# Performance work log

Hardware: AMD Instinct MI355X
Metric: run time of the kernel (lower is better)

Reference implementation:

```python
import jax, jax.numpy as jnp
import numpy as np

G, N, E = 64, 2048, 32768      # graphs, nodes/graph, edges/graph
D, H, O, L = 128, 128, 2, 3    # node_dim, hid_dim, out_dim, max_layer
ALL = 500_000                  # global feature table rows


def setup_inputs() -> dict:
    key = jax.random.key(0)
    ks = jax.random.split(key, 12)
    s = 1.0 / np.sqrt(D)  # D == H so one scale suffices
    return {
        "all_features": jax.random.normal(ks[0], (ALL, D), jnp.float32),
        "feature_index": jax.random.randint(ks[1], (G, N), 0, ALL),
        "edge_index": jax.random.randint(ks[2], (G, 2, E), 0, N),
        "action": 2,  # uses action+1 = 3 GCN layers
        "lin_res_w": jax.random.normal(ks[3], (D, H), jnp.float32) * s,
        "lin_res_b": jnp.zeros((H,), jnp.float32),
        "gcn_w": jax.random.normal(ks[4], (L, H, H), jnp.float32) * s,
        "gcn_b": jnp.zeros((L, H), jnp.float32),
        "fc1_w": jax.random.normal(ks[5], (H, H), jnp.float32) * s,
        "fc1_b": jnp.zeros((H,), jnp.float32),
        "lin_w": jax.random.normal(ks[6], (H, O), jnp.float32) * s,
        "lin_b": jnp.zeros((O,), jnp.float32),
    }


def _gcn_conv(x, src, dst, W, b):
    """PyG GCNConv: add self-loops, symmetric deg^-1/2 norm, scatter-add."""
    n = x.shape[0]
    h = x @ W                                             # [N,H]
    loop = jnp.arange(n)
    src2 = jnp.concatenate([src, loop])
    dst2 = jnp.concatenate([dst, loop])
    deg = jax.ops.segment_sum(jnp.ones_like(dst2, dtype=h.dtype), dst2,
                              num_segments=n)             # >=1 via self-loops
    dinv = jax.lax.rsqrt(deg)
    coef = dinv[src2] * dinv[dst2]                        # [E+N]
    out = jax.ops.segment_sum(h[src2] * coef[:, None], dst2, num_segments=n)
    return out + b


def reference(all_features, feature_index, edge_index, action,
              lin_res_w, lin_res_b, gcn_w, gcn_b,
              fc1_w, fc1_b, lin_w, lin_b):
    n_layers = int(action) + 1

    def per_graph(feats, src, dst):
        # residual branch (dropout is identity in eval mode)
        x1 = jax.nn.relu(feats @ lin_res_w + lin_res_b)   # [N,H]
        x = feats
        for k in range(n_layers):
            x = jax.nn.relu(_gcn_conv(x, src, dst, gcn_w[k], gcn_b[k]))
        x = jax.nn.relu((x + x1) @ fc1_w + fc1_b)
        return jnp.mean(x, axis=0)                        # [H]

    feats = all_features[feature_index]                   # [G,N,D] gather
    target_feats = jax.vmap(per_graph)(feats, edge_index[:, 0], edge_index[:, 1])
    logits = target_feats @ lin_w + lin_b                 # [G,O]
    return jax.nn.log_softmax(logits, axis=1), logits
```

## Files before the change

kernel.cpp:

```cpp
#include <hip/hip_runtime.h>

#define G 64
#define N 2048
#define E 32768
#define GN (G*N)
#define PADR 36

typedef __attribute__((ext_vector_type(8))) short bf16x8;
typedef __attribute__((ext_vector_type(4))) float f32x4;

__device__ __forceinline__ float4 ld4(const float* p) { return *reinterpret_cast<const float4*>(p); }
__device__ __forceinline__ unsigned short f2bf(float x) {
    unsigned u = __float_as_uint(x);
    u += 0x7FFF + ((u >> 16) & 1);
    return (unsigned short)(u >> 16);
}
__device__ __forceinline__ unsigned pack2(float a, float b) {
    return (unsigned)f2bf(a) | ((unsigned)f2bf(b) << 16);
}
__device__ __forceinline__ float bflo(unsigned u) { return __uint_as_float(u << 16); }
__device__ __forceinline__ float bfhi(unsigned u) { return __uint_as_float(u & 0xFFFF0000u); }
__device__ __forceinline__ float bfs(short s) { return __uint_as_float(((unsigned)(unsigned short)s) << 16); }

__device__ __forceinline__ int swz(int bid, int chunk) { return (bid & 7) * chunk + (bid >> 3); }

__global__ __launch_bounds__(1024) void k_init(const int* __restrict__ ei,
        float* __restrict__ dinv, int* __restrict__ perm, int* __restrict__ rankg,
        int* __restrict__ sdeg, float* __restrict__ sdinv, int* __restrict__ lvlG,
        const float* __restrict__ wres, const float* __restrict__ gw,
        const float* __restrict__ wfc, unsigned short* __restrict__ Wt,
        float* __restrict__ tgt) {
    int t = threadIdx.x;
    if (blockIdx.x == G + 40) {
        #pragma unroll
        for (int j = 0; j < 8; ++j) tgt[j*1024 + t] = 0.f;
        return;
    }
    if (blockIdx.x >= G) {
        if (t >= 256) return;
        int pb = blockIdx.x - G;
        int m = pb >> 3;
        int tid = (pb & 7) * 256 + t;
        const float* src = (m == 0) ? wres : (m < 4 ? gw + (size_t)(m-1)*16384 : wfc);
        int c = tid >> 4, q = tid & 15;
        float v[8];
        #pragma unroll
        for (int j = 0; j < 8; ++j) v[j] = src[(q*8 + j)*128 + c];
        uint4 p;
        p.x = pack2(v[0], v[1]); p.y = pack2(v[2], v[3]);
        p.z = pack2(v[4], v[5]); p.w = pack2(v[6], v[7]);
        *reinterpret_cast<uint4*>(Wt + (size_t)m*16384 + c*128 + ((q ^ (c & 7)) << 3)) = p;
        return;
    }
    int g = blockIdx.x;
    __shared__ int scnt[2048];
    __shared__ int hist[128];
    __shared__ int basev[129];
    __shared__ int lvl[128];
    __shared__ int ctr[128];
    scnt[t] = 0; scnt[t + 1024] = 0;
    if (t < 128) { hist[t] = 0; ctr[t] = 0; }
    __syncthreads();
    const int* dstp = ei + (size_t)g*2*E + E;
    for (int e = t; e < E; e += 1024) atomicAdd(&scnt[dstp[e]], 1);
    __syncthreads();
    int a = scnt[2*t], b = scnt[2*t + 1];
    dinv[(g<<11) + 2*t]     = rsqrtf((float)(a + 1));
    dinv[(g<<11) + 2*t + 1] = rsqrtf((float)(b + 1));
    int ba = min(a, 127), bb = min(b, 127);
    atomicAdd(&hist[ba], 1);
    atomicAdd(&hist[bb], 1);
    __syncthreads();
    if (t == 0) {
        int suf = 0;
        basev[128] = 0;
        for (int d = 127; d >= 0; --d) { suf += hist[d]; basev[d] = suf; }
        int run = 0;
        for (int i = 0; i < 128; ++i) { lvl[i] = run; run += basev[i + 1]; }
    }
    __syncthreads();
    {
        int sa = basev[ba + 1] + atomicAdd(&ctr[ba], 1);
        perm[(g<<11) + sa] = 2*t;
        sdeg[(g<<11) + sa] = a;
        sdinv[(g<<11) + sa] = rsqrtf((float)(a + 1));
        rankg[(g<<11) + 2*t] = sa;
        int sb = basev[bb + 1] + atomicAdd(&ctr[bb], 1);
        perm[(g<<11) + sb] = 2*t + 1;
        sdeg[(g<<11) + sb] = b;
        sdinv[(g<<11) + sb] = rsqrtf((float)(b + 1));
        rankg[(g<<11) + 2*t + 1] = sb;
    }
    if (t < 128) lvlG[g*128 + t] = lvl[t];
}

__global__ __launch_bounds__(512) void k_gemm_g2(const int* __restrict__ fidx,
        const float* __restrict__ tab, const unsigned short* __restrict__ Wt,
        const float* __restrict__ bres, const float* __restrict__ dinv,
        unsigned short* __restrict__ X1, unsigned short* __restrict__ Hb,
        const int* __restrict__ ei, const int* __restrict__ rankg,
        const int* __restrict__ lvlG, int* __restrict__ padj) {
    __shared__ unsigned short sW[2*16384];
    const int t = threadIdx.x;

    if (blockIdx.x < G) {
        int* cur   = reinterpret_cast<int*>(sW);
        int* rankL = cur + 2048;
        int* lvlL  = rankL + 2048;
        int g = blockIdx.x;
        #pragma unroll
        for (int i = 0; i < 4; ++i) {
            cur[i*512 + t] = 0;
            rankL[i*512 + t] = rankg[(g<<11) + i*512 + t];
        }
        if (t < 128) lvlL[t] = lvlG[g*128 + t];
        __syncthreads();
        const int* srcp = ei + (size_t)g*2*E;
        const int* dstp = srcp + E;
        for (int e = t; e < E; e += 512) {
            int dst = dstp[e];
            int i = atomicAdd(&cur[dst], 1);
            padj[(size_t)g*E + lvlL[i] + rankL[dst]] = srcp[e];
        }
        return;
    }

    {
        const float4* s = reinterpret_cast<const float4*>(Wt);
        float4* d = reinterpret_cast<float4*>(sW);
        #pragma unroll
        for (int i = 0; i < 8; ++i) d[i*512 + t] = s[i*512 + t];
    }
    __syncthreads();

    const int lane = t & 63, w = t >> 6;
    const int wrow = (w & 3) << 6;
    const int wcol = (w >> 2) << 6;
    const size_t row0 = (size_t)swz(blockIdx.x - G, GN/256/8) * 256;
    const int l15 = lane & 15, l4 = lane >> 4;

    size_t rbase[4];
    const float* rowp[4];
    #pragma unroll
    for (int f2 = 0; f2 < 4; ++f2) {
        rbase[f2] = row0 + wrow + f2*16 + l15;
        rowp[f2] = tab + (size_t)fidx[rbase[f2]] * 128;
    }

    f32x4 acc0[4][4], acc1[4][4];
    #pragma unroll
    for (int i = 0; i < 4; ++i)
        #pragma unroll
        for (int j = 0; j < 4; ++j) {
            acc0[i][j] = (f32x4){0.f, 0.f, 0.f, 0.f};
            acc1[i][j] = (f32x4){0.f, 0.f, 0.f, 0.f};
        }

    #pragma unroll
    for (int kk = 0; kk < 4; ++kk) {
        bf16x8 xf[4];
        #pragma unroll
        for (int f2 = 0; f2 < 4; ++f2) {
            int col = (kk << 5) + (l4 << 3);
            float4 u = ld4(rowp[f2] + col);
            float4 v = ld4(rowp[f2] + col + 4);
            bf16x8 r;
            r[0] = (short)f2bf(u.x); r[1] = (short)f2bf(u.y);
            r[2] = (short)f2bf(u.z); r[3] = (short)f2bf(u.w);
            r[4] = (short)f2bf(v.x); r[5] = (short)f2bf(v.y);
            r[6] = (short)f2bf(v.z); r[7] = (short)f2bf(v.w);
            xf[f2] = r;
        }
        #pragma unroll
        for (int f = 0; f < 4; ++f) {
            int c = wcol + f*16 + l15;
            int off = c*128 + (((kk*4 + l4) ^ (c & 7)) << 3);
            bf16x8 wf0 = *reinterpret_cast<const bf16x8*>(&sW[off]);
            bf16x8 wf1 = *reinterpret_cast<const bf16x8*>(&sW[16384 + off]);
            #pragma unroll
            for (int f2 = 0; f2 < 4; ++f2) {
                acc0[f2][f] = __builtin_amdgcn_mfma_f32_16x16x32_bf16(wf0, xf[f2], acc0[f2][f], 0, 0, 0);
                acc1[f2][f] = __builtin_amdgcn_mfma_f32_16x16x32_bf16(wf1, xf[f2], acc1[f2][f], 0, 0, 0);
            }
        }
    }

    float dv[4];
    #pragma unroll
    for (int f2 = 0; f2 < 4; ++f2) dv[f2] = dinv[rbase[f2]];

    #pragma unroll
    for (int f = 0; f < 4; ++f) {
        int colb = wcol + f*16 + (l4 << 2);
        float4 bs = ld4(bres + colb);
        #pragma unroll
        for (int f2 = 0; f2 < 4; ++f2) {
            f32x4 v0 = acc0[f2][f];
            uint2 p0;
            p0.x = pack2(fmaxf(v0[0] + bs.x, 0.f), fmaxf(v0[1] + bs.y, 0.f));
            p0.y = pack2(fmaxf(v0[2] + bs.z, 0.f), fmaxf(v0[3] + bs.w, 0.f));
            *reinterpret_cast<uint2*>(X1 + (rbase[f2] << 7) + colb) = p0;
            f32x4 v1 = acc1[f2][f];
            float d = dv[f2];
            uint2 p1;
            p1.x = pack2(v1[0]*d, v1[1]*d);
            p1.y = pack2(v1[2]*d, v1[3]*d);
            *reinterpret_cast<uint2*>(Hb + (rbase[f2] << 7) + colb) = p1;
        }
    }
}

template<int MODE>
__global__ __launch_bounds__(512) void k_gemm(const unsigned short* __restrict__ A,
        const unsigned short* __restrict__ A2, const unsigned short* __restrict__ Wt,
        const float* __restrict__ bias, const float* __restrict__ dinv,
        unsigned short* __restrict__ C, float* __restrict__ tgt) {
    __shared__ unsigned short sW[16384];
    const int t = threadIdx.x;
    {
        const float4* s = reinterpret_cast<const float4*>(Wt);
        float4* d = reinterpret_cast<float4*>(sW);
        #pragma unroll
        for (int i = 0; i < 4; ++i) d[i*512 + t] = s[i*512 + t];
    }
    __syncthreads();

    const int lane = t & 63, w = t >> 6;
    const int wrow = (w & 3) << 6;
    const int wcol = (w >> 2) << 6;
    const size_t row0 = (size_t)swz(blockIdx.x, GN/256/8) * 256;
    const int l15 = lane & 15, l4 = lane >> 4;

    size_t rbase[4];
    #pragma unroll
    for (int f2 = 0; f2 < 4; ++f2) rbase[f2] = row0 + wrow + f2*16 + l15;

    f32x4 acc[4][4];
    #pragma unroll
    for (int i = 0; i < 4; ++i)
        #pragma unroll
        for (int j = 0; j < 4; ++j) acc[i][j] = (f32x4){0.f, 0.f, 0.f, 0.f};

    #pragma unroll
    for (int kk = 0; kk < 4; ++kk) {
        bf16x8 xf[4];
        #pragma unroll
        for (int f2 = 0; f2 < 4; ++f2) {
            const unsigned short* ap = A + (rbase[f2] << 7) + (kk << 5) + (l4 << 3);
            if (MODE == 2) {
                bf16x8 x = *reinterpret_cast<const bf16x8*>(ap);
                bf16x8 y = *reinterpret_cast<const bf16x8*>(A2 + (rbase[f2] << 7) + (kk << 5) + (l4 << 3));
                bf16x8 r;
                #pragma unroll
                for (int j = 0; j < 8; ++j) r[j] = (short)f2bf(bfs(x[j]) + bfs(y[j]));
                xf[f2] = r;
            } else {
                xf[f2] = *reinterpret_cast<const bf16x8*>(ap);
            }
        }
        #pragma unroll
        for (int f = 0; f < 4; ++f) {
            int c = wcol + f*16 + l15;
            int off = c*128 + (((kk*4 + l4) ^ (c & 7)) << 3);
            bf16x8 wf = *reinterpret_cast<const bf16x8*>(&sW[off]);
            #pragma unroll
            for (int f2 = 0; f2 < 4; ++f2)
                acc[f2][f] = __builtin_amdgcn_mfma_f32_16x16x32_bf16(wf, xf[f2], acc[f2][f], 0, 0, 0);
        }
    }

    if (MODE == 2) {
        float cs[4][4];
        #pragma unroll
        for (int f = 0; f < 4; ++f) {
            int colb = wcol + f*16 + (l4 << 2);
            float4 bs = ld4(bias + colb);
            #pragma unroll
            for (int j = 0; j < 4; ++j) cs[f][j] = 0.f;
            #pragma unroll
            for (int f2 = 0; f2 < 4; ++f2) {
                cs[f][0] += fmaxf(acc[f2][f][0] + bs.x, 0.f);
                cs[f][1] += fmaxf(acc[f2][f][1] + bs.y, 0.f);
                cs[f][2] += fmaxf(acc[f2][f][2] + bs.z, 0.f);
                cs[f][3] += fmaxf(acc[f2][f][3] + bs.w, 0.f);
            }
        }
        #pragma unroll
        for (int d = 1; d < 16; d <<= 1)
            #pragma unroll
            for (int f = 0; f < 4; ++f)
                #pragma unroll
                for (int j = 0; j < 4; ++j)
                    cs[f][j] += __shfl_xor(cs[f][j], d);
        if (l15 == 0) {
            int g = (int)(row0 >> 11);
            #pragma unroll
            for (int f = 0; f < 4; ++f)
                #pragma unroll
                for (int j = 0; j < 4; ++j)
                    atomicAdd(&tgt[g*128 + wcol + f*16 + (l4 << 2) + j], cs[f][j]);
        }
        return;
    }

    float dv[4];
    #pragma unroll
    for (int f2 = 0; f2 < 4; ++f2) dv[f2] = dinv[rbase[f2]];
    #pragma unroll
    for (int f = 0; f < 4; ++f) {
        int colb = wcol + f*16 + (l4 << 2);
        #pragma unroll
        for (int f2 = 0; f2 < 4; ++f2) {
            f32x4 v = acc[f2][f];
            float d = dv[f2];
            uint2 p; p.x = pack2(v[0]*d, v[1]*d); p.y = pack2(v[2]*d, v[3]*d);
            *reinterpret_cast<uint2*>(C + (rbase[f2] << 7) + colb) = p;
        }
    }
}

__global__ __launch_bounds__(1024) void k_agg(const unsigned short* __restrict__ h,
        const int* __restrict__ padj, const int* __restrict__ lvlG,
        const int* __restrict__ perm, const int* __restrict__ sdeg,
        const float* __restrict__ sdinv, const float* __restrict__ bias,
        unsigned short* __restrict__ out) {
    __shared__ unsigned short sIN[2048 * PADR];
    __shared__ int lvlL[128];
    const int t = threadIdx.x;
    const int g  = blockIdx.x >> 2;
    const int c0 = (blockIdx.x & 3) << 5;
    const unsigned short* hg = h + (((size_t)g << 11) << 7) + c0;

    if (t < 128) lvlL[t] = lvlG[g*128 + t];
    {
        int r0 = t >> 3;
        int j  = t & 7;
        for (int i = 0; i < 16; ++i) {
            int r = r0 + (i << 7);
            uint2 v = *reinterpret_cast<const uint2*>(hg + ((size_t)r << 7) + j*4);
            *reinterpret_cast<uint2*>(&sIN[r*PADR + j*4]) = v;
        }
    }
    __syncthreads();

    const int* pa = padj + (size_t)g*E;
    float bs[32];
    #pragma unroll
    for (int q = 0; q < 8; ++q) {
        float4 b4 = ld4(bias + c0 + q*4);
        bs[q*4] = b4.x; bs[q*4+1] = b4.y; bs[q*4+2] = b4.z; bs[q*4+3] = b4.w;
    }

    #pragma unroll
    for (int half = 0; half < 2; ++half) {
        const int r = t + (half << 10);
        const int n  = perm[(g << 11) + r];
        const int dg = sdeg[(g << 11) + r];
        const float dv = sdinv[(g << 11) + r];
        float acc[32];
        {
            const unsigned short* rp = &sIN[n*PADR];
            #pragma unroll
            for (int q = 0; q < 8; ++q) {
                uint2 u = *reinterpret_cast<const uint2*>(rp + q*4);
                acc[q*4]   = bflo(u.x); acc[q*4+1] = bfhi(u.x);
                acc[q*4+2] = bflo(u.y); acc[q*4+3] = bfhi(u.y);
            }
        }
        int i = 0;
        for (; i + 2 <= dg; i += 2) {
            int s0 = pa[lvlL[i] + r];
            int s1 = pa[lvlL[i+1] + r];
            const unsigned short* rp0 = &sIN[s0*PADR];
            const unsigned short* rp1 = &sIN[s1*PADR];
            uint2 u0[8], u1[8];
            #pragma unroll
            for (int q = 0; q < 8; ++q) u0[q] = *reinterpret_cast<const uint2*>(rp0 + q*4);
            #pragma unroll
            for (int q = 0; q < 8; ++q) u1[q] = *reinterpret_cast<const uint2*>(rp1 + q*4);
            #pragma unroll
            for (int q = 0; q < 8; ++q) {
                acc[q*4]   += bflo(u0[q].x) + bflo(u1[q].x);
                acc[q*4+1] += bfhi(u0[q].x) + bfhi(u1[q].x);
                acc[q*4+2] += bflo(u0[q].y) + bflo(u1[q].y);
                acc[q*4+3] += bfhi(u0[q].y) + bfhi(u1[q].y);
            }
        }
        if (i < dg) {
            int s = pa[lvlL[i] + r];
            const unsigned short* rp = &sIN[s*PADR];
            #pragma unroll
            for (int q = 0; q < 8; ++q) {
                uint2 u = *reinterpret_cast<const uint2*>(rp + q*4);
                acc[q*4]   += bflo(u.x); acc[q*4+1] += bfhi(u.x);
                acc[q*4+2] += bflo(u.y); acc[q*4+3] += bfhi(u.y);
            }
        }
        unsigned short* op = out + (((size_t)(g << 11) + n) << 7) + c0;
        uint4 o0, o1;
        o0.x = pack2(fmaxf(acc[0]*dv+bs[0],0.f),  fmaxf(acc[1]*dv+bs[1],0.f));
        o0.y = pack2(fmaxf(acc[2]*dv+bs[2],0.f),  fmaxf(acc[3]*dv+bs[3],0.f));
        o0.z = pack2(fmaxf(acc[4]*dv+bs[4],0.f),  fmaxf(acc[5]*dv+bs[5],0.f));
        o0.w = pack2(fmaxf(acc[6]*dv+bs[6],0.f),  fmaxf(acc[7]*dv+bs[7],0.f));
        o1.x = pack2(fmaxf(acc[8]*dv+bs[8],0.f),  fmaxf(acc[9]*dv+bs[9],0.f));
        o1.y = pack2(fmaxf(acc[10]*dv+bs[10],0.f),fmaxf(acc[11]*dv+bs[11],0.f));
        o1.z = pack2(fmaxf(acc[12]*dv+bs[12],0.f),fmaxf(acc[13]*dv+bs[13],0.f));
        o1.w = pack2(fmaxf(acc[14]*dv+bs[14],0.f),fmaxf(acc[15]*dv+bs[15],0.f));
        *reinterpret_cast<uint4*>(op) = o0;
        *reinterpret_cast<uint4*>(op + 8) = o1;
        uint4 o2, o3;
        o2.x = pack2(fmaxf(acc[16]*dv+bs[16],0.f),fmaxf(acc[17]*dv+bs[17],0.f));
        o2.y = pack2(fmaxf(acc[18]*dv+bs[18],0.f),fmaxf(acc[19]*dv+bs[19],0.f));
        o2.z = pack2(fmaxf(acc[20]*dv+bs[20],0.f),fmaxf(acc[21]*dv+bs[21],0.f));
        o2.w = pack2(fmaxf(acc[22]*dv+bs[22],0.f),fmaxf(acc[23]*dv+bs[23],0.f));
        o3.x = pack2(fmaxf(acc[24]*dv+bs[24],0.f),fmaxf(acc[25]*dv+bs[25],0.f));
        o3.y = pack2(fmaxf(acc[26]*dv+bs[26],0.f),fmaxf(acc[27]*dv+bs[27],0.f));
        o3.z = pack2(fmaxf(acc[28]*dv+bs[28],0.f),fmaxf(acc[29]*dv+bs[29],0.f));
        o3.w = pack2(fmaxf(acc[30]*dv+bs[30],0.f),fmaxf(acc[31]*dv+bs[31],0.f));
        *reinterpret_cast<uint4*>(op + 16) = o2;
        *reinterpret_cast<uint4*>(op + 24) = o3;
    }
}

__global__ __launch_bounds__(64) void k_final(const float* __restrict__ tgt,
        const float* __restrict__ lw, const float* __restrict__ lb, float* __restrict__ outp) {
    int g = blockIdx.x, lane = threadIdx.x;
    float l0 = 0.f, l1 = 0.f;
    #pragma unroll
    for (int c = lane; c < 128; c += 64) {
        float v = tgt[g*128 + c] * (1.0f/2048.0f);
        l0 += v * lw[c*2];
        l1 += v * lw[c*2 + 1];
    }
    #pragma unroll
    for (int d = 32; d; d >>= 1) { l0 += __shfl_xor(l0, d); l1 += __shfl_xor(l1, d); }
    if (lane == 0) {
        l0 += lb[0]; l1 += lb[1];
        float m = fmaxf(l0, l1);
        float lse = m + logf(expf(l0 - m) + expf(l1 - m));
        outp[g*2]         = l0 - lse;
        outp[g*2 + 1]     = l1 - lse;
        outp[G*2 + g*2]     = l0;
        outp[G*2 + g*2 + 1] = l1;
    }
}

extern "C" void kernel_launch(void* const* d_in, const int* in_sizes, int n_in,
                              void* d_out, int out_size, void* d_ws, size_t ws_size,
                              hipStream_t stream) {
    const float* all_features = (const float*)d_in[0];
    const int*   fidx = (const int*)d_in[1];
    const int*   ei   = (const int*)d_in[2];
    const float* wres = (const float*)d_in[4];
    const float* bres = (const float*)d_in[5];
    const float* gw   = (const float*)d_in[6];
    const float* gb   = (const float*)d_in[7];
    const float* wfc  = (const float*)d_in[8];
    const float* bfc  = (const float*)d_in[9];
    const float* lw   = (const float*)d_in[10];
    const float* lb   = (const float*)d_in[11];
    float* out = (float*)d_out;

    char* ws = (char*)d_ws;
    size_t o = 0;
    auto alloc = [&](size_t bytes) { char* p = ws + o; o += (bytes + 255) & ~(size_t)255; return p; };
    unsigned short* X  = (unsigned short*)alloc((size_t)GN*128*2);
    unsigned short* Hb = (unsigned short*)alloc((size_t)GN*128*2);
    unsigned short* X1 = (unsigned short*)alloc((size_t)GN*128*2);
    unsigned short* Wt = (unsigned short*)alloc((size_t)5*16384*2);
    int*   padj  = (int*)alloc((size_t)G*E*4);
    int*   lvlG  = (int*)alloc((size_t)G*128*4);
    int*   perm  = (int*)alloc((size_t)GN*4);
    int*   rankg = (int*)alloc((size_t)GN*4);
    int*   sdeg  = (int*)alloc((size_t)GN*4);
    float* sdinv = (float*)alloc((size_t)GN*4);
    float* dinv  = (float*)alloc((size_t)GN*4);
    float* tgt   = (float*)alloc((size_t)G*128*4);

    k_init<<<G + 41, 1024, 0, stream>>>(ei, dinv, perm, rankg, sdeg, sdinv, lvlG,
                                        wres, gw, wfc, Wt, tgt);

    k_gemm_g2<<<G + GN/256, 512, 0, stream>>>(fidx, all_features, Wt, bres, dinv, X1, Hb,
                                              ei, rankg, lvlG, padj);

    k_agg<<<G*4, 1024, 0, stream>>>(Hb, padj, lvlG, perm, sdeg, sdinv, gb, X);
    for (int l = 1; l < 3; ++l) {
        k_gemm<1><<<GN/256, 512, 0, stream>>>(X, nullptr, Wt + (size_t)(1+l)*16384, nullptr, dinv, Hb, nullptr);
        k_agg<<<G*4, 1024, 0, stream>>>(Hb, padj, lvlG, perm, sdeg, sdinv, gb + (size_t)l*128, X);
    }

    k_gemm<2><<<GN/256, 512, 0, stream>>>(X, X1, Wt + (size_t)4*16384, bfc, nullptr, nullptr, tgt);

    k_final<<<G, 64, 0, stream>>>(tgt, lw, lb, out);
}
```

Baseline: 268.8 us.

## Fuse per-layer GEMM into GCN aggregation kernel for layers two and three

Each block now multiplies its graph's full node tile by a 32-column slice of the layer weight using MFMA, scales by dinv and writes the result straight into the shared-memory staging buffer. It then runs the neighbour aggregation from LDS, so the separate GEMM kernel and its global write and read of the hidden tensor disappear for layers 2 and 3. The trade-off is that each of the four column blocks per graph reads the whole input row set (4x redundant X reads) and holds fewer rows per MFMA wave. Launch count drops by two.

```diff
diff --git a/kernel.cpp b/kernel.cpp
--- a/kernel.cpp
+++ b/kernel.cpp
@@ -210,11 +210,9 @@
     }
 }
 
-template<int MODE>
-__global__ __launch_bounds__(512) void k_gemm(const unsigned short* __restrict__ A,
+__global__ __launch_bounds__(512) void k_gemm2(const unsigned short* __restrict__ A,
         const unsigned short* __restrict__ A2, const unsigned short* __restrict__ Wt,
-        const float* __restrict__ bias, const float* __restrict__ dinv,
-        unsigned short* __restrict__ C, float* __restrict__ tgt) {
+        const float* __restrict__ bias, float* __restrict__ tgt) {
     __shared__ unsigned short sW[16384];
     const int t = threadIdx.x;
     {
@@ -247,16 +245,12 @@
         #pragma unroll
         for (int f2 = 0; f2 < 4; ++f2) {
             const unsigned short* ap = A + (rbase[f2] << 7) + (kk << 5) + (l4 << 3);
-            if (MODE == 2) {
-                bf16x8 x = *reinterpret_cast<const bf16x8*>(ap);
-                bf16x8 y = *reinterpret_cast<const bf16x8*>(A2 + (rbase[f2] << 7) + (kk << 5) + (l4 << 3));
-                bf16x8 r;
-                #pragma unroll
-                for (int j = 0; j < 8; ++j) r[j] = (short)f2bf(bfs(x[j]) + bfs(y[j]));
-                xf[f2] = r;
-            } else {
-                xf[f2] = *reinterpret_cast<const bf16x8*>(ap);
-            }
+            bf16x8 x = *reinterpret_cast<const bf16x8*>(ap);
+            bf16x8 y = *reinterpret_cast<const bf16x8*>(A2 + (rbase[f2] << 7) + (kk << 5) + (l4 << 3));
+            bf16x8 r;
+            #pragma unroll
+            for (int j = 0; j < 8; ++j) r[j] = (short)f2bf(bfs(x[j]) + bfs(y[j]));
+            xf[f2] = r;
         }
         #pragma unroll
         for (int f = 0; f < 4; ++f) {
@@ -269,53 +263,35 @@
         }
     }
 
-    if (MODE == 2) {
-        float cs[4][4];
-        #pragma unroll
-        for (int f = 0; f < 4; ++f) {
-            int colb = wcol + f*16 + (l4 << 2);
-            float4 bs = ld4(bias + colb);
-            #pragma unroll
-            for (int j = 0; j < 4; ++j) cs[f][j] = 0.f;
-            #pragma unroll
-            for (int f2 = 0; f2 < 4; ++f2) {
-                cs[f][0] += fmaxf(acc[f2][f][0] + bs.x, 0.f);
-                cs[f][1] += fmaxf(acc[f2][f][1] + bs.y, 0.f);
-                cs[f][2] += fmaxf(acc[f2][f][2] + bs.z, 0.f);
-                cs[f][3] += fmaxf(acc[f2][f][3] + bs.w, 0.f);
-            }
-        }
-        #pragma unroll
-        for (int d = 1; d < 16; d <<= 1)
-            #pragma unroll
-            for (int f = 0; f < 4; ++f)
-                #pragma unroll
-                for (int j = 0; j < 4; ++j)
-                    cs[f][j] += __shfl_xor(cs[f][j], d);
-        if (l15 == 0) {
-            int g = (int)(row0 >> 11);
-            #pragma unroll
-            for (int f = 0; f < 4; ++f)
-                #pragma unroll
-                for (int j = 0; j < 4; ++j)
-                    atomicAdd(&tgt[g*128 + wcol + f*16 + (l4 << 2) + j], cs[f][j]);
-        }
-        return;
-    }
-
-    float dv[4];
-    #pragma unroll
-    for (int f2 = 0; f2 < 4; ++f2) dv[f2] = dinv[rbase[f2]];
+    float cs[4][4];
     #pragma unroll
     for (int f = 0; f < 4; ++f) {
         int colb = wcol + f*16 + (l4 << 2);
+        float4 bs = ld4(bias + colb);
+        #pragma unroll
+        for (int j = 0; j < 4; ++j) cs[f][j] = 0.f;
         #pragma unroll
         for (int f2 = 0; f2 < 4; ++f2) {
-            f32x4 v = acc[f2][f];
-            float d = dv[f2];
-            uint2 p; p.x = pack2(v[0]*d, v[1]*d); p.y = pack2(v[2]*d, v[3]*d);
-            *reinterpret_cast<uint2*>(C + (rbase[f2] << 7) + colb) = p;
-        }
+            cs[f][0] += fmaxf(acc[f2][f][0] + bs.x, 0.f);
+            cs[f][1] += fmaxf(acc[f2][f][1] + bs.y, 0.f);
+            cs[f][2] += fmaxf(acc[f2][f][2] + bs.z, 0.f);
+            cs[f][3] += fmaxf(acc[f2][f][3] + bs.w, 0.f);
+        }
+    }
+    #pragma unroll
+    for (int d = 1; d < 16; d <<= 1)
+        #pragma unroll
+        for (int f = 0; f < 4; ++f)
+            #pragma unroll
+            for (int j = 0; j < 4; ++j)
+                cs[f][j] += __shfl_xor(cs[f][j], d);
+    if (l15 == 0) {
+        int g = (int)(row0 >> 11);
+        #pragma unroll
+        for (int f = 0; f < 4; ++f)
+            #pragma unroll
+            for (int j = 0; j < 4; ++j)
+                atomicAdd(&tgt[g*128 + wcol + f*16 + (l4 << 2) + j], cs[f][j]);
     }
 }
 
@@ -422,6 +398,135 @@
     }
 }
 
+__global__ __launch_bounds__(1024) void k_fused(const unsigned short* __restrict__ Xin,
+        const unsigned short* __restrict__ WtL,
+        const int* __restrict__ padj, const int* __restrict__ lvlG,
+        const int* __restrict__ perm, const int* __restrict__ sdeg,
+        const float* __restrict__ sdinv, const float* __restrict__ dinv,
+        const float* __restrict__ bias,
+        unsigned short* __restrict__ Xout) {
+    __shared__ unsigned short sIN[2048 * PADR];
+    __shared__ int lvlL[128];
+    const int t = threadIdx.x;
+    const int wg = swz(blockIdx.x, 32);
+    const int g  = wg >> 2;
+    const int c0 = (wg & 3) << 5;
+
+    if (t < 128) lvlL[t] = lvlG[g*128 + t];
+
+    const int lane = t & 63, wv = t >> 6;
+    const int l15 = lane & 15, l4 = lane >> 4;
+
+    bf16x8 wf[2][4];
+    #pragma unroll
+    for (int f = 0; f < 2; ++f) {
+        int c = c0 + f*16 + l15;
+        #pragma unroll
+        for (int kk = 0; kk < 4; ++kk)
+            wf[f][kk] = *reinterpret_cast<const bf16x8*>(&WtL[c*128 + (((kk*4 + l4) ^ (c & 7)) << 3)]);
+    }
+
+    const unsigned short* xg = Xin + (((size_t)g << 11) << 7);
+    #pragma unroll
+    for (int rt = 0; rt < 8; ++rt) {
+        int rowb = ((wv << 3) + rt) << 4;
+        int row = rowb + l15;
+        f32x4 acc0 = (f32x4){0.f,0.f,0.f,0.f};
+        f32x4 acc1 = (f32x4){0.f,0.f,0.f,0.f};
+        #pragma unroll
+        for (int kk = 0; kk < 4; ++kk) {
+            bf16x8 xf = *reinterpret_cast<const bf16x8*>(xg + ((size_t)row << 7) + (kk << 5) + (l4 << 3));
+            acc0 = __builtin_amdgcn_mfma_f32_16x16x32_bf16(wf[0][kk], xf, acc0, 0, 0, 0);
+            acc1 = __builtin_amdgcn_mfma_f32_16x16x32_bf16(wf[1][kk], xf, acc1, 0, 0, 0);
+        }
+        float d = dinv[(g << 11) + row];
+        uint2 p0, p1;
+        p0.x = pack2(acc0[0]*d, acc0[1]*d); p0.y = pack2(acc0[2]*d, acc0[3]*d);
+        p1.x = pack2(acc1[0]*d, acc1[1]*d); p1.y = pack2(acc1[2]*d, acc1[3]*d);
+        *reinterpret_cast<uint2*>(&sIN[row*PADR + (l4 << 2)])      = p0;
+        *reinterpret_cast<uint2*>(&sIN[row*PADR + 16 + (l4 << 2)]) = p1;
+    }
+    __syncthreads();
+
+    const int* pa = padj + (size_t)g*E;
+    float bs[32];
+    #pragma unroll
+    for (int q = 0; q < 8; ++q) {
+        float4 b4 = ld4(bias + c0 + q*4);
+        bs[q*4] = b4.x; bs[q*4+1] = b4.y; bs[q*4+2] = b4.z; bs[q*4+3] = b4.w;
+    }
+
+    #pragma unroll
+    for (int half = 0; half < 2; ++half) {
+        const int r = t + (half << 10);
+        const int n  = perm[(g << 11) + r];
+        const int dg = sdeg[(g << 11) + r];
+        const float dv = sdinv[(g << 11) + r];
+        float acc[32];
+        {
+            const unsigned short* rp = &sIN[n*PADR];
+            #pragma unroll
+            for (int q = 0; q < 8; ++q) {
+                uint2 u = *reinterpret_cast<const uint2*>(rp + q*4);
+                acc[q*4]   = bflo(u.x); acc[q*4+1] = bfhi(u.x);
+                acc[q*4+2] = bflo(u.y); acc[q*4+3] = bfhi(u.y);
+            }
+        }
+        int i = 0;
+        for (; i + 2 <= dg; i += 2) {
+            int s0 = pa[lvlL[i] + r];
+            int s1 = pa[lvlL[i+1] + r];
+            const unsigned short* rp0 = &sIN[s0*PADR];
+            const unsigned short* rp1 = &sIN[s1*PADR];
+            uint2 u0[8], u1[8];
+            #pragma unroll
+            for (int q = 0; q < 8; ++q) u0[q] = *reinterpret_cast<const uint2*>(rp0 + q*4);
+            #pragma unroll
+            for (int q = 0; q < 8; ++q) u1[q] = *reinterpret_cast<const uint2*>(rp1 + q*4);
+            #pragma unroll
+            for (int q = 0; q < 8; ++q) {
+                acc[q*4]   += bflo(u0[q].x) + bflo(u1[q].x);
+                acc[q*4+1] += bfhi(u0[q].x) + bfhi(u1[q].x);
+                acc[q*4+2] += bflo(u0[q].y) + bflo(u1[q].y);
+                acc[q*4+3] += bfhi(u0[q].y) + bfhi(u1[q].y);
+            }
+        }
+        if (i < dg) {
+            int s = pa[lvlL[i] + r];
+            const unsigned short* rp = &sIN[s*PADR];
+            #pragma unroll
+            for (int q = 0; q < 8; ++q) {
+                uint2 u = *reinterpret_cast<const uint2*>(rp + q*4);
+                acc[q*4]   += bflo(u.x); acc[q*4+1] += bfhi(u.x);
+                acc[q*4+2] += bflo(u.y); acc[q*4+3] += bfhi(u.y);
+            }
+        }
+        unsigned short* op = Xout + (((size_t)(g << 11) + n) << 7) + c0;
+        uint4 o0, o1;
+        o0.x = pack2(fmaxf(acc[0]*dv+bs[0],0.f),  fmaxf(acc[1]*dv+bs[1],0.f));
+        o0.y = pack2(fmaxf(acc[2]*dv+bs[2],0.f),  fmaxf(acc[3]*dv+bs[3],0.f));
+        o0.z = pack2(fmaxf(acc[4]*dv+bs[4],0.f),  fmaxf(acc[5]*dv+bs[5],0.f));
+        o0.w = pack2(fmaxf(acc[6]*dv+bs[6],0.f),  fmaxf(acc[7]*dv+bs[7],0.f));
+        o1.x = pack2(fmaxf(acc[8]*dv+bs[8],0.f),  fmaxf(acc[9]*dv+bs[9],0.f));
+        o1.y = pack2(fmaxf(acc[10]*dv+bs[10],0.f),fmaxf(acc[11]*dv+bs[11],0.f));
+        o1.z = pack2(fmaxf(acc[12]*dv+bs[12],0.f),fmaxf(acc[13]*dv+bs[13],0.f));
+        o1.w = pack2(fmaxf(acc[14]*dv+bs[14],0.f),fmaxf(acc[15]*dv+bs[15],0.f));
+        *reinterpret_cast<uint4*>(op) = o0;
+        *reinterpret_cast<uint4*>(op + 8) = o1;
+        uint4 o2, o3;
+        o2.x = pack2(fmaxf(acc[16]*dv+bs[16],0.f),fmaxf(acc[17]*dv+bs[17],0.f));
+        o2.y = pack2(fmaxf(acc[18]*dv+bs[18],0.f),fmaxf(acc[19]*dv+bs[19],0.f));
+        o2.z = pack2(fmaxf(acc[20]*dv+bs[20],0.f),fmaxf(acc[21]*dv+bs[21],0.f));
+        o2.w = pack2(fmaxf(acc[22]*dv+bs[22],0.f),fmaxf(acc[23]*dv+bs[23],0.f));
+        o3.x = pack2(fmaxf(acc[24]*dv+bs[24],0.f),fmaxf(acc[25]*dv+bs[25],0.f));
+        o3.y = pack2(fmaxf(acc[26]*dv+bs[26],0.f),fmaxf(acc[27]*dv+bs[27],0.f));
+        o3.z = pack2(fmaxf(acc[28]*dv+bs[28],0.f),fmaxf(acc[29]*dv+bs[29],0.f));
+        o3.w = pack2(fmaxf(acc[30]*dv+bs[30],0.f),fmaxf(acc[31]*dv+bs[31],0.f));
+        *reinterpret_cast<uint4*>(op + 16) = o2;
+        *reinterpret_cast<uint4*>(op + 24) = o3;
+    }
+}
+
 __global__ __launch_bounds__(64) void k_final(const float* __restrict__ tgt,
         const float* __restrict__ lw, const float* __restrict__ lb, float* __restrict__ outp) {
     int g = blockIdx.x, lane = threadIdx.x;
@@ -465,7 +570,7 @@
     size_t o = 0;
     auto alloc = [&](size_t bytes) { char* p = ws + o; o += (bytes + 255) & ~(size_t)255; return p; };
     unsigned short* X  = (unsigned short*)alloc((size_t)GN*128*2);
-    unsigned short* Hb = (unsigned short*)alloc((size_t)GN*128*2);
+    unsigned short* Xb = (unsigned short*)alloc((size_t)GN*128*2);
     unsigned short* X1 = (unsigned short*)alloc((size_t)GN*128*2);
     unsigned short* Wt = (unsigned short*)alloc((size_t)5*16384*2);
     int*   padj  = (int*)alloc((size_t)G*E*4);
@@ -480,16 +585,16 @@
     k_init<<<G + 41, 1024, 0, stream>>>(ei, dinv, perm, rankg, sdeg, sdinv, lvlG,
                                         wres, gw, wfc, Wt, tgt);
 
-    k_gemm_g2<<<G + GN/256, 512, 0, stream>>>(fidx, all_features, Wt, bres, dinv, X1, Hb,
+    k_gemm_g2<<<G + GN/256, 512, 0, stream>>>(fidx, all_features, Wt, bres, dinv, X1, Xb,
                                               ei, rankg, lvlG, padj);
 
-    k_agg<<<G*4, 1024, 0, stream>>>(Hb, padj, lvlG, perm, sdeg, sdinv, gb, X);
-    for (int l = 1; l < 3; ++l) {
-        k_gemm<1><<<GN/256, 512, 0, stream>>>(X, nullptr, Wt + (size_t)(1+l)*16384, nullptr, dinv, Hb, nullptr);
-        k_agg<<<G*4, 1024, 0, stream>>>(Hb, padj, lvlG, perm, sdeg, sdinv, gb + (size_t)l*128, X);
-    }
-
-    k_gemm<2><<<GN/256, 512, 0, stream>>>(X, X1, Wt + (size_t)4*16384, bfc, nullptr, nullptr, tgt);
+    k_agg<<<G*4, 1024, 0, stream>>>(Xb, padj, lvlG, perm, sdeg, sdinv, gb, X);
+    k_fused<<<G*4, 1024, 0, stream>>>(X, Wt + (size_t)2*16384, padj, lvlG, perm, sdeg, sdinv,
+                                      dinv, gb + 128, Xb);
+    k_fused<<<G*4, 1024, 0, stream>>>(Xb, Wt + (size_t)3*16384, padj, lvlG, perm, sdeg, sdinv,
+                                      dinv, gb + 256, X);
+
+    k_gemm2<<<GN/256, 512, 0, stream>>>(X, X1, Wt + (size_t)4*16384, bfc, tgt);
 
     k_final<<<G, 64, 0, stream>>>(tgt, lw, lb, out);
 }
```

Measured after the change: 243.6 us. -9.4%, faster.

## Fuse per-layer GCN weight GEMM into aggregation kernel, eliminating Hb round-trip

Applied to the files above, without the earlier changes.

Each GCN layer's feature transform (X@W scaled by dinv) now runs inside the aggregation kernel. Each block computes its 32-column slice of H for the whole graph straight into shared memory, so the separate GEMM launches and the global Hb write and read go away. For the first layer the block also gathers rows from the feature table itself, so k_gemm_g2 now only computes the residual branch. The cost is redundancy: each of the four column-slice blocks per graph re-reads the full input rows (four times for the table gather) and recomputes its part of the GEMM at lower MFMA density. Separate ping-pong buffers keep layer input and output from aliasing.

```diff
diff --git a/kernel.cpp b/kernel.cpp
--- a/kernel.cpp
+++ b/kernel.cpp
@@ -96,11 +96,11 @@
 
 __global__ __launch_bounds__(512) void k_gemm_g2(const int* __restrict__ fidx,
         const float* __restrict__ tab, const unsigned short* __restrict__ Wt,
-        const float* __restrict__ bres, const float* __restrict__ dinv,
-        unsigned short* __restrict__ X1, unsigned short* __restrict__ Hb,
+        const float* __restrict__ bres,
+        unsigned short* __restrict__ X1,
         const int* __restrict__ ei, const int* __restrict__ rankg,
         const int* __restrict__ lvlG, int* __restrict__ padj) {
-    __shared__ unsigned short sW[2*16384];
+    __shared__ unsigned short sW[16384];
     const int t = threadIdx.x;
 
     if (blockIdx.x < G) {
@@ -129,7 +129,7 @@
         const float4* s = reinterpret_cast<const float4*>(Wt);
         float4* d = reinterpret_cast<float4*>(sW);
         #pragma unroll
-        for (int i = 0; i < 8; ++i) d[i*512 + t] = s[i*512 + t];
+        for (int i = 0; i < 4; ++i) d[i*512 + t] = s[i*512 + t];
     }
     __syncthreads();
 
@@ -147,14 +147,11 @@
         rowp[f2] = tab + (size_t)fidx[rbase[f2]] * 128;
     }
 
-    f32x4 acc0[4][4], acc1[4][4];
+    f32x4 acc0[4][4];
     #pragma unroll
     for (int i = 0; i < 4; ++i)
         #pragma unroll
-        for (int j = 0; j < 4; ++j) {
-            acc0[i][j] = (f32x4){0.f, 0.f, 0.f, 0.f};
-            acc1[i][j] = (f32x4){0.f, 0.f, 0.f, 0.f};
-        }
+        for (int j = 0; j < 4; ++j) acc0[i][j] = (f32x4){0.f, 0.f, 0.f, 0.f};
 
     #pragma unroll
     for (int kk = 0; kk < 4; ++kk) {
@@ -176,18 +173,11 @@
             int c = wcol + f*16 + l15;
             int off = c*128 + (((kk*4 + l4) ^ (c & 7)) << 3);
             bf16x8 wf0 = *reinterpret_cast<const bf16x8*>(&sW[off]);
-            bf16x8 wf1 = *reinterpret_cast<const bf16x8*>(&sW[16384 + off]);
-            #pragma unroll
-            for (int f2 = 0; f2 < 4; ++f2) {
+            #pragma unroll
+            for (int f2 = 0; f2 < 4; ++f2)
                 acc0[f2][f] = __builtin_amdgcn_mfma_f32_16x16x32_bf16(wf0, xf[f2], acc0[f2][f], 0, 0, 0);
-                acc1[f2][f] = __builtin_amdgcn_mfma_f32_16x16x32_bf16(wf1, xf[f2], acc1[f2][f], 0, 0, 0);
-            }
-        }
-    }
-
-    float dv[4];
-    #pragma unroll
-    for (int f2 = 0; f2 < 4; ++f2) dv[f2] = dinv[rbase[f2]];
+        }
+    }
 
     #pragma unroll
     for (int f = 0; f < 4; ++f) {
@@ -200,21 +190,13 @@
             p0.x = pack2(fmaxf(v0[0] + bs.x, 0.f), fmaxf(v0[1] + bs.y, 0.f));
             p0.y = pack2(fmaxf(v0[2] + bs.z, 0.f), fmaxf(v0[3] + bs.w, 0.f));
             *reinterpret_cast<uint2*>(X1 + (rbase[f2] << 7) + colb) = p0;
-            f32x4 v1 = acc1[f2][f];
-            float d = dv[f2];
-            uint2 p1;
-            p1.x = pack2(v1[0]*d, v1[1]*d);
-            p1.y = pack2(v1[2]*d, v1[3]*d);
-            *reinterpret_cast<uint2*>(Hb + (rbase[f2] << 7) + colb) = p1;
-        }
-    }
-}
-
-template<int MODE>
-__global__ __launch_bounds__(512) void k_gemm(const unsigned short* __restrict__ A,
+        }
+    }
+}
+
+__global__ __launch_bounds__(512) void k_gemm2(const unsigned short* __restrict__ A,
         const unsigned short* __restrict__ A2, const unsigned short* __restrict__ Wt,
-        const float* __restrict__ bias, const float* __restrict__ dinv,
-        unsigned short* __restrict__ C, float* __restrict__ tgt) {
+        const float* __restrict__ bias, float* __restrict__ tgt) {
     __shared__ unsigned short sW[16384];
     const int t = threadIdx.x;
     {
@@ -247,16 +229,12 @@
         #pragma unroll
         for (int f2 = 0; f2 < 4; ++f2) {
             const unsigned short* ap = A + (rbase[f2] << 7) + (kk << 5) + (l4 << 3);
-            if (MODE == 2) {
-                bf16x8 x = *reinterpret_cast<const bf16x8*>(ap);
-                bf16x8 y = *reinterpret_cast<const bf16x8*>(A2 + (rbase[f2] << 7) + (kk << 5) + (l4 << 3));
-                bf16x8 r;
-                #pragma unroll
-                for (int j = 0; j < 8; ++j) r[j] = (short)f2bf(bfs(x[j]) + bfs(y[j]));
-                xf[f2] = r;
-            } else {
-                xf[f2] = *reinterpret_cast<const bf16x8*>(ap);
-            }
+            bf16x8 x = *reinterpret_cast<const bf16x8*>(ap);
+            bf16x8 y = *reinterpret_cast<const bf16x8*>(A2 + (rbase[f2] << 7) + (kk << 5) + (l4 << 3));
+            bf16x8 r;
+            #pragma unroll
+            for (int j = 0; j < 8; ++j) r[j] = (short)f2bf(bfs(x[j]) + bfs(y[j]));
+            xf[f2] = r;
         }
         #pragma unroll
         for (int f = 0; f < 4; ++f) {
@@ -269,77 +247,99 @@
         }
     }
 
-    if (MODE == 2) {
-        float cs[4][4];
-        #pragma unroll
-        for (int f = 0; f < 4; ++f) {
-            int colb = wcol + f*16 + (l4 << 2);
-            float4 bs = ld4(bias + colb);
-            #pragma unroll
-            for (int j = 0; j < 4; ++j) cs[f][j] = 0.f;
-            #pragma unroll
-            for (int f2 = 0; f2 < 4; ++f2) {
-                cs[f][0] += fmaxf(acc[f2][f][0] + bs.x, 0.f);
-                cs[f][1] += fmaxf(acc[f2][f][1] + bs.y, 0.f);
-                cs[f][2] += fmaxf(acc[f2][f][2] + bs.z, 0.f);
-                cs[f][3] += fmaxf(acc[f2][f][3] + bs.w, 0.f);
-            }
-        }
-        #pragma unroll
-        for (int d = 1; d < 16; d <<= 1)
-            #pragma unroll
-            for (int f = 0; f < 4; ++f)
-                #pragma unroll
-                for (int j = 0; j < 4; ++j)
-                    cs[f][j] += __shfl_xor(cs[f][j], d);
-        if (l15 == 0) {
-            int g = (int)(row0 >> 11);
-            #pragma unroll
-            for (int f = 0; f < 4; ++f)
-                #pragma unroll
-                for (int j = 0; j < 4; ++j)
-                    atomicAdd(&tgt[g*128 + wcol + f*16 + (l4 << 2) + j], cs[f][j]);
-        }
-        return;
-    }
-
-    float dv[4];
-    #pragma unroll
-    for (int f2 = 0; f2 < 4; ++f2) dv[f2] = dinv[rbase[f2]];
+    float cs[4][4];
     #pragma unroll
     for (int f = 0; f < 4; ++f) {
         int colb = wcol + f*16 + (l4 << 2);
+        float4 bs = ld4(bias + colb);
+        #pragma unroll
+        for (int j = 0; j < 4; ++j) cs[f][j] = 0.f;
         #pragma unroll
         for (int f2 = 0; f2 < 4; ++f2) {
-            f32x4 v = acc[f2][f];
-            float d = dv[f2];
-            uint2 p; p.x = pack2(v[0]*d, v[1]*d); p.y = pack2(v[2]*d, v[3]*d);
-            *reinterpret_cast<uint2*>(C + (rbase[f2] << 7) + colb) = p;
-        }
-    }
-}
-
-__global__ __launch_bounds__(1024) void k_agg(const unsigned short* __restrict__ h,
+            cs[f][0] += fmaxf(acc[f2][f][0] + bs.x, 0.f);
+            cs[f][1] += fmaxf(acc[f2][f][1] + bs.y, 0.f);
+            cs[f][2] += fmaxf(acc[f2][f][2] + bs.z, 0.f);
+            cs[f][3] += fmaxf(acc[f2][f][3] + bs.w, 0.f);
+        }
+    }
+    #pragma unroll
+    for (int d = 1; d < 16; d <<= 1)
+        #pragma unroll
+        for (int f = 0; f < 4; ++f)
+            #pragma unroll
+            for (int j = 0; j < 4; ++j)
+                cs[f][j] += __shfl_xor(cs[f][j], d);
+    if (l15 == 0) {
+        int g = (int)(row0 >> 11);
+        #pragma unroll
+        for (int f = 0; f < 4; ++f)
+            #pragma unroll
+            for (int j = 0; j < 4; ++j)
+                atomicAdd(&tgt[g*128 + wcol + f*16 + (l4 << 2) + j], cs[f][j]);
+    }
+}
+
+template<int GATHER>
+__global__ __launch_bounds__(1024) void k_fused(const unsigned short* __restrict__ Xin,
+        const int* __restrict__ fidx, const float* __restrict__ tab,
+        const unsigned short* __restrict__ WtL,
         const int* __restrict__ padj, const int* __restrict__ lvlG,
         const int* __restrict__ perm, const int* __restrict__ sdeg,
-        const float* __restrict__ sdinv, const float* __restrict__ bias,
-        unsigned short* __restrict__ out) {
+        const float* __restrict__ sdinv, const float* __restrict__ dinv,
+        const float* __restrict__ bias,
+        unsigned short* __restrict__ Xout) {
     __shared__ unsigned short sIN[2048 * PADR];
     __shared__ int lvlL[128];
     const int t = threadIdx.x;
-    const int g  = blockIdx.x >> 2;
-    const int c0 = (blockIdx.x & 3) << 5;
-    const unsigned short* hg = h + (((size_t)g << 11) << 7) + c0;
+    const int wg = swz(blockIdx.x, 32);
+    const int g  = wg >> 2;
+    const int c0 = (wg & 3) << 5;
 
     if (t < 128) lvlL[t] = lvlG[g*128 + t];
-    {
-        int r0 = t >> 3;
-        int j  = t & 7;
-        for (int i = 0; i < 16; ++i) {
-            int r = r0 + (i << 7);
-            uint2 v = *reinterpret_cast<const uint2*>(hg + ((size_t)r << 7) + j*4);
-            *reinterpret_cast<uint2*>(&sIN[r*PADR + j*4]) = v;
-        }
+
+    const int lane = t & 63, wv = t >> 6;
+    const int l15 = lane & 15, l4 = lane >> 4;
+
+    bf16x8 wf[2][4];
+    #pragma unroll
+    for (int f = 0; f < 2; ++f) {
+        int c = c0 + f*16 + l15;
+        #pragma unroll
+        for (int kk = 0; kk < 4; ++kk)
+            wf[f][kk] = *reinterpret_cast<const bf16x8*>(&WtL[c*128 + (((kk*4 + l4) ^ (c & 7)) << 3)]);
+    }
+
+    const unsigned short* xg = (GATHER ? nullptr : Xin + (((size_t)g << 11) << 7));
+    #pragma unroll
+    for (int rt = 0; rt < 8; ++rt) {
+        int row = (((wv << 3) + rt) << 4) + l15;
+        f32x4 acc0 = (f32x4){0.f,0.f,0.f,0.f};
+        f32x4 acc1 = (f32x4){0.f,0.f,0.f,0.f};
+        const float* gp;
+        if (GATHER) gp = tab + (size_t)fidx[(g << 11) + row] * 128;
+        #pragma unroll
+        for (int kk = 0; kk < 4; ++kk) {
+            bf16x8 xf;
+            if (GATHER) {
+                int col = (kk << 5) + (l4 << 3);
+                float4 u = ld4(gp + col);
+                float4 v = ld4(gp + col + 4);
+                xf[0] = (short)f2bf(u.x); xf[1] = (short)f2bf(u.y);
+                xf[2] = (short)f2bf(u.z); xf[3] = (short)f2bf(u.w);
+                xf[4] = (short)f2bf(v.x); xf[5] = (short)f2bf(v.y);
+                xf[6] = (short)f2bf(v.z); xf[7] = (short)f2bf(v.w);
+            } else {
+                xf = *reinterpret_cast<const bf16x8*>(xg + ((size_t)row << 7) + (kk << 5) + (l4 << 3));
+            }
+            acc0 = __builtin_amdgcn_mfma_f32_16x16x32_bf16(wf[0][kk], xf, acc0, 0, 0, 0);
+            acc1 = __builtin_amdgcn_mfma_f32_16x16x32_bf16(wf[1][kk], xf, acc1, 0, 0, 0);
+        }
+        float d = dinv[(g << 11) + row];
+        uint2 p0, p1;
+        p0.x = pack2(acc0[0]*d, acc0[1]*d); p0.y = pack2(acc0[2]*d, acc0[3]*d);
+        p1.x = pack2(acc1[0]*d, acc1[1]*d); p1.y = pack2(acc1[2]*d, acc1[3]*d);
+        *reinterpret_cast<uint2*>(&sIN[row*PADR + (l4 << 2)])      = p0;
+        *reinterpret_cast<uint2*>(&sIN[row*PADR + 16 + (l4 << 2)]) = p1;
     }
     __syncthreads();
 
@@ -396,7 +396,7 @@
                 acc[q*4+2] += bflo(u.y); acc[q*4+3] += bfhi(u.y);
             }
         }
-        unsigned short* op = out + (((size_t)(g << 11) + n) << 7) + c0;
+        unsigned short* op = Xout + (((size_t)(g << 11) + n) << 7) + c0;
         uint4 o0, o1;
         o0.x = pack2(fmaxf(acc[0]*dv+bs[0],0.f),  fmaxf(acc[1]*dv+bs[1],0.f));
         o0.y = pack2(fmaxf(acc[2]*dv+bs[2],0.f),  fmaxf(acc[3]*dv+bs[3],0.f));
@@ -465,7 +465,7 @@
     size_t o = 0;
     auto alloc = [&](size_t bytes) { char* p = ws + o; o += (bytes + 255) & ~(size_t)255; return p; };
     unsigned short* X  = (unsigned short*)alloc((size_t)GN*128*2);
-    unsigned short* Hb = (unsigned short*)alloc((size_t)GN*128*2);
+    unsigned short* Xb = (unsigned short*)alloc((size_t)GN*128*2);
     unsigned short* X1 = (unsigned short*)alloc((size_t)GN*128*2);
     unsigned short* Wt = (unsigned short*)alloc((size_t)5*16384*2);
     int*   padj  = (int*)alloc((size_t)G*E*4);
@@ -480,16 +480,17 @@
     k_init<<<G + 41, 1024, 0, stream>>>(ei, dinv, perm, rankg, sdeg, sdinv, lvlG,
                                         wres, gw, wfc, Wt, tgt);
 
-    k_gemm_g2<<<G + GN/256, 512, 0, stream>>>(fidx, all_features, Wt, bres, dinv, X1, Hb,
+    k_gemm_g2<<<G + GN/256, 512, 0, stream>>>(fidx, all_features, Wt, bres, X1,
                                               ei, rankg, lvlG, padj);
 
-    k_agg<<<G*4, 1024, 0, stream>>>(Hb, padj, lvlG, perm, sdeg, sdinv, gb, X);
-    for (int l = 1; l < 3; ++l) {
-        k_gemm<1><<<GN/256, 512, 0, stream>>>(X, nullptr, Wt + (size_t)(1+l)*16384, nullptr, dinv, Hb, nullptr);
-        k_agg<<<G*4, 1024, 0, stream>>>(Hb, padj, lvlG, perm, sdeg, sdinv, gb + (size_t)l*128, X);
-    }
-
-    k_gemm<2><<<GN/256, 512, 0, stream>>>(X, X1, Wt + (size_t)4*16384, bfc, nullptr, nullptr, tgt);
+    k_fused<1><<<G*4, 1024, 0, stream>>>(nullptr, fidx, all_features, Wt + (size_t)16384,
+                                         padj, lvlG, perm, sdeg, sdinv, dinv, gb, X);
+    k_fused<0><<<G*4, 1024, 0, stream>>>(X, nullptr, nullptr, Wt + (size_t)2*16384,
+                                         padj, lvlG, perm, sdeg, sdinv, dinv, gb + 128, Xb);
+    k_fused<0><<<G*4, 1024, 0, stream>>>(Xb, nullptr, nullptr, Wt + (size_t)3*16384,
+                                         padj, lvlG, perm, sdeg, sdinv, dinv, gb + 256, X);
+
+    k_gemm2<<<GN/256, 512, 0, stream>>>(X, X1, Wt + (size_t)4*16384, bfc, tgt);
 
     k_final<<<G, 64, 0, stream>>>(tgt, lw, lb, out);
 }
```

After: 260.5 us. 1.03x faster.
